# Performance work log

Hardware: AMD Instinct MI355X
Metric: run time of the kernel (lower is better)

The kernel has to match this reference:

```python
import jax, jax.numpy as jnp
import numpy as np

WIN = (8, 8)
NUM_HEADS = 6


def bchw_to_bnc(x, win):
    B, C, H, W = x.shape
    SH, SW = win
    oh, ow = H // SH, W // SW
    # B,C,oh,SH,ow,SW -> B,oh,ow,SH,SW,C -> (B*oh*ow, SH*SW, C)
    x = x.reshape(B, C, oh, SH, ow, SW)
    x = jnp.transpose(x, (0, 2, 4, 3, 5, 1))
    return x.reshape(B * oh * ow, SH * SW, C)


def bnc_to_bchw(x, out_shape, win):
    OB, OC, OH, OW = out_shape
    SH, SW = win
    oh, ow = OH // SH, OW // SW
    C = x.shape[-1]
    x = x.reshape(OB, oh, ow, SH, SW, C)
    x = jnp.transpose(x, (0, 5, 1, 3, 2, 4))
    return x.reshape(OB, C, OH, OW)


def setup_inputs() -> dict:
    key = jax.random.key(0)
    k1, k2, k3 = jax.random.split(key, 3)
    B, C, H, W = 4, 192, 384, 384
    x = jax.random.normal(k1, (B, C, H, W), dtype=jnp.float32)
    # MHA params: qkv_proj Linear(C, 3C), head_proj Linear(C, C)
    qkv_w = jax.random.normal(k2, (3 * C, C), dtype=jnp.float32) * 0.02
    qkv_b = jnp.zeros((3 * C,), dtype=jnp.float32)
    head_w = jax.random.normal(k3, (C, C), dtype=jnp.float32) * 0.02
    head_b = jnp.zeros((C,), dtype=jnp.float32)
    return {"x": x, "qkv_w": qkv_w, "qkv_b": qkv_b, "head_w": head_w, "head_b": head_b}


def reference(x, qkv_w, qkv_b, head_w, head_b):
    out_shape = x.shape
    C = x.shape[1]
    H = NUM_HEADS
    D = C // H  # head dim
    # window partition: (Bw, N, C) with N = 64
    t = bchw_to_bnc(x, WIN)
    # QKV projection
    qkv = t @ qkv_w.T + qkv_b  # (Bw, N, 3C)
    q, k, v = jnp.split(qkv, 3, axis=-1)
    Bw, N, _ = q.shape
    q = q.reshape(Bw, N, H, D).transpose(0, 2, 1, 3)  # bhnd
    k = k.reshape(Bw, N, H, D).transpose(0, 2, 1, 3)
    v = v.reshape(Bw, N, H, D).transpose(0, 2, 1, 3)
    scale = 1.0 / jnp.sqrt(jnp.asarray(D, dtype=q.dtype))
    scores = jnp.einsum('bhqd,bhkd->bhqk', q, k) * scale
    attn = jax.nn.softmax(scores, axis=-1)
    o = jnp.einsum('bhqk,bhkd->bhqd', attn, v)
    o = o.transpose(0, 2, 1, 3).reshape(Bw, N, C)
    o = o @ head_w.T + head_b
    return bnc_to_bchw(o, out_shape, WIN)
```

## Files before the change

kernel.cpp:

```cpp
#include <hip/hip_runtime.h>
#include <hip/hip_bf16.h>

typedef __attribute__((ext_vector_type(8))) short short8;
typedef __attribute__((ext_vector_type(4))) float f32x4;

#if __has_builtin(__builtin_amdgcn_exp2f)
#define EXP2F(x) __builtin_amdgcn_exp2f(x)
#else
#define EXP2F(x) exp2f(x)
#endif
#if __has_builtin(__builtin_amdgcn_rcpf)
#define RCPF(x) __builtin_amdgcn_rcpf(x)
#else
#define RCPF(x) (1.0f/(x))
#endif

#define SQ 208
#define SV 144

#define LDS_TOTAL 66048

__device__ __forceinline__ unsigned short f2bf(float f) {
    union { float f; unsigned u; } v; v.f = f;
    unsigned r = v.u + 0x7FFFu + ((v.u >> 16) & 1u);
    return (unsigned short)(r >> 16);
}
__device__ __forceinline__ unsigned pk2(float lo, float hi) {
    __hip_bfloat162 h = __float22bfloat162_rn(make_float2(lo, hi));
    union { __hip_bfloat162 h; unsigned u; } cv;
    cv.h = h;
    return cv.u;
}

__global__ void cvt_weights(const float* __restrict__ qw, const float* __restrict__ hw,
                            unsigned short* __restrict__ wq, unsigned short* __restrict__ wh) {
    int i = blockIdx.x * 256 + threadIdx.x;
    if (i < 576 * 192) wq[i] = f2bf(qw[i]);
    if (i < 192 * 192) wh[i] = f2bf(hw[i]);
}

__global__ __launch_bounds__(256, 2) void wmha(
    const float* __restrict__ x, const float* __restrict__ qkv_b,
    const float* __restrict__ head_b, const unsigned short* __restrict__ wq,
    const unsigned short* __restrict__ whc, float* __restrict__ out)
{
    extern __shared__ char smem[];
    char* const x_lds = smem;
    char* const o_lds = smem;
    char* const q_lds = smem + 25600;
    char* const k_lds = smem + 38912;
    char* const v_lds = smem + 52224;

    const int tid = threadIdx.x;
    const int ln  = tid & 15;
    const int hi4 = (tid >> 4) & 3;
    const int wid = tid >> 6;
    char* const p_scr = smem + 13312 + wid * 2304;

    const int bid  = blockIdx.x;
    const int widx = (bid & 7) * 1152 + (bid >> 3);
    const int b  = widx / 2304;
    const int rr = widx % 2304;
    const int oy = rr / 48, ox = rr % 48;
    const int row0 = oy * 8, col0 = ox * 8;

    auto ldwf = [&](int g, int mt, short8* wf) {
        const int hl = mt / 6, sec = (mt % 6) >> 1, e = mt & 1;
        const int r0 = sec * 192 + (3 * g + hl) * 32 + e * 16;
        #pragma unroll
        for (int kt = 0; kt < 6; ++kt)
            wf[kt] = *(const short8*)(wq + (r0 + ln) * 192 + kt * 32 + hi4 * 8);
    };

    short8 wf0[6];
    ldwf(0, wid, wf0);

    {
        const int tok = tid & 63;
        const int qd  = tid >> 6;
        const int y = tok >> 3, xx = tok & 7;
        const float* gp = x + ((size_t)(b * 192) * 384 + (row0 + y)) * 384 + (col0 + xx);
        char* wp = x_lds + tok * 400 + qd * 96;
        #pragma unroll
        for (int kk = 0; kk < 12; ++kk) {
            const int c = qd * 48 + kk * 4;
            float f0 = gp[(size_t)(c + 0) * 147456];
            float f1 = gp[(size_t)(c + 1) * 147456];
            float f2 = gp[(size_t)(c + 2) * 147456];
            float f3 = gp[(size_t)(c + 3) * 147456];
            uint2 u;
            u.x = pk2(f0, f1);
            u.y = pk2(f2, f3);
            *(uint2*)(wp + kk * 8) = u;
        }
    }
    __syncthreads();

    short8 bx[4][6];

    f32x4 acc[3][4];
    #pragma unroll
    for (int mm = 0; mm < 3; ++mm)
        #pragma unroll
        for (int nt = 0; nt < 4; ++nt)
            acc[mm][nt] = (f32x4){0.f, 0.f, 0.f, 0.f};

    const float SC2 = 0.25503417f;

    auto qkv_do = [&](int g, int mt, const short8* wf) {
        const int hl = mt / 6, sec = (mt % 6) >> 1, e = mt & 1;
        const int r0 = sec * 192 + (3 * g + hl) * 32 + e * 16;
        if (sec < 2) {
            char* dst = (sec == 0) ? q_lds : k_lds;
            const float4 bias = *(const float4*)(qkv_b + r0 + hi4 * 4);
            #pragma unroll
            for (int nt = 0; nt < 4; ++nt) {
                f32x4 a = {bias.x, bias.y, bias.z, bias.w};
                #pragma unroll
                for (int kt = 0; kt < 6; ++kt)
                    a = __builtin_amdgcn_mfma_f32_16x16x32_bf16(wf[kt], bx[nt][kt], a, 0, 0, 0);
                uint2 u;
                u.x = pk2(a[0], a[1]);
                u.y = pk2(a[2], a[3]);
                *(uint2*)(dst + (nt * 16 + ln) * SQ + hl * 64 + (e * 16 + hi4 * 4) * 2) = u;
            }
        } else {
            const float bv = qkv_b[r0 + ln];
            #pragma unroll
            for (int nt = 0; nt < 4; ++nt) {
                f32x4 a = {bv, bv, bv, bv};
                #pragma unroll
                for (int kt = 0; kt < 6; ++kt)
                    a = __builtin_amdgcn_mfma_f32_16x16x32_bf16(bx[nt][kt], wf[kt], a, 0, 0, 0);
                uint2 u;
                u.x = pk2(a[0], a[1]);
                u.y = pk2(a[2], a[3]);
                *(uint2*)(v_lds + (hl * 32 + e * 16 + ln) * SV + (nt * 16 + hi4 * 4) * 2) = u;
            }
        }
    };

    auto attn = [&](int g) {
        #pragma unroll
        for (int uu = 0; uu < 3; ++uu) {
            const int u = wid + uu * 4;
            const int hl = u >> 2, i0 = (u & 3) * 16;
            const short8 bq = *(const short8*)(q_lds + (i0 + ln) * SQ + hl * 64 + hi4 * 16);
            f32x4 s[4];
            #pragma unroll
            for (int kt = 0; kt < 4; ++kt) {
                const short8 ak = *(const short8*)(k_lds + (kt * 16 + ln) * SQ + hl * 64 + hi4 * 16);
                f32x4 z = {0.f, 0.f, 0.f, 0.f};
                s[kt] = __builtin_amdgcn_mfma_f32_16x16x32_bf16(ak, bq, z, 0, 0, 0);
            }
            float sum = 0.f;
            #pragma unroll
            for (int kt = 0; kt < 4; ++kt)
                #pragma unroll
                for (int r = 0; r < 4; ++r) {
                    s[kt][r] = EXP2F(s[kt][r] * SC2);
                    sum += s[kt][r];
                }
            sum += __shfl_xor(sum, 16);
            sum += __shfl_xor(sum, 32);
            const float rinv = RCPF(sum);
            #pragma unroll
            for (int kt = 0; kt < 4; ++kt) {
                uint2 u2;
                u2.x = pk2(s[kt][0], s[kt][1]);
                u2.y = pk2(s[kt][2], s[kt][3]);
                *(uint2*)(p_scr + ln * SV + kt * 32 + hi4 * 8) = u2;
            }
            short8 pf[2];
            #pragma unroll
            for (int kc = 0; kc < 2; ++kc)
                pf[kc] = *(const short8*)(p_scr + ln * SV + kc * 64 + hi4 * 16);
            #pragma unroll
            for (int dt = 0; dt < 2; ++dt) {
                f32x4 o = {0.f, 0.f, 0.f, 0.f};
                #pragma unroll
                for (int kc = 0; kc < 2; ++kc) {
                    const short8 av = *(const short8*)(v_lds + (hl * 32 + dt * 16 + ln) * SV + kc * 64 + hi4 * 16);
                    o = __builtin_amdgcn_mfma_f32_16x16x32_bf16(av, pf[kc], o, 0, 0, 0);
                }
                uint2 u2;
                u2.x = pk2(o[0] * rinv, o[1] * rinv);
                u2.y = pk2(o[2] * rinv, o[3] * rinv);
                *(uint2*)(o_lds + (i0 + ln) * SQ + hl * 64 + (dt * 16 + hi4 * 4) * 2) = u2;
            }
        }
    };

    auto proj = [&](int g) {
        short8 bo[4][3];
        #pragma unroll
        for (int nt = 0; nt < 4; ++nt)
            #pragma unroll
            for (int kt = 0; kt < 3; ++kt)
                bo[nt][kt] = *(const short8*)(o_lds + (nt * 16 + ln) * SQ + kt * 64 + hi4 * 16);
        #pragma unroll
        for (int mm = 0; mm < 3; ++mm) {
            const int c0 = (wid * 3 + mm) * 16;
            short8 af[3];
            #pragma unroll
            for (int kt = 0; kt < 3; ++kt)
                af[kt] = *(const short8*)(whc + (c0 + ln) * 192 + g * 96 + kt * 32 + hi4 * 8);
            #pragma unroll
            for (int nt = 0; nt < 4; ++nt)
                #pragma unroll
                for (int kt = 0; kt < 3; ++kt)
                    acc[mm][nt] = __builtin_amdgcn_mfma_f32_16x16x32_bf16(af[kt], bo[nt][kt], acc[mm][nt], 0, 0, 0);
        }
    };

    #pragma unroll
    for (int nt = 0; nt < 4; ++nt)
        #pragma unroll
        for (int kt = 0; kt < 6; ++kt)
            bx[nt][kt] = *(const short8*)(x_lds + (nt * 16 + ln) * 400 + kt * 64 + hi4 * 16);
    qkv_do(0, wid, wf0);
    for (int mt = wid + 4; mt < 18; mt += 4) {
        short8 wf[6];
        ldwf(0, mt, wf);
        qkv_do(0, mt, wf);
    }
    __syncthreads();
    attn(0);
    __syncthreads();
    proj(0);
    for (int mt = wid; mt < 18; mt += 4) {
        short8 wf[6];
        ldwf(1, mt, wf);
        qkv_do(1, mt, wf);
    }
    __syncthreads();
    attn(1);
    __syncthreads();
    proj(1);

    #pragma unroll
    for (int mm = 0; mm < 3; ++mm) {
        const int c0 = (wid * 3 + mm) * 16;
        const float4 hb = *(const float4*)(head_b + c0 + hi4 * 4);
        #pragma unroll
        for (int nt = 0; nt < 4; ++nt) {
            const int tt = nt * 16 + ln;
            const int y = tt >> 3, xx = tt & 7;
            float* op = out + ((size_t)(b * 192) * 384 + (row0 + y)) * 384 + (col0 + xx);
            op[(size_t)(c0 + hi4 * 4 + 0) * 147456] = acc[mm][nt][0] + hb.x;
            op[(size_t)(c0 + hi4 * 4 + 1) * 147456] = acc[mm][nt][1] + hb.y;
            op[(size_t)(c0 + hi4 * 4 + 2) * 147456] = acc[mm][nt][2] + hb.z;
            op[(size_t)(c0 + hi4 * 4 + 3) * 147456] = acc[mm][nt][3] + hb.w;
        }
    }
}

extern "C" void kernel_launch(void* const* d_in, const int* in_sizes, int n_in,
                              void* d_out, int out_size, void* d_ws, size_t ws_size,
                              hipStream_t stream) {
    const float* x      = (const float*)d_in[0];
    const float* qkv_w  = (const float*)d_in[1];
    const float* qkv_b  = (const float*)d_in[2];
    const float* head_w = (const float*)d_in[3];
    const float* head_b = (const float*)d_in[4];
    float* out = (float*)d_out;

    unsigned short* wq  = (unsigned short*)d_ws;
    unsigned short* whc = wq + 576 * 192;

    cvt_weights<<<432, 256, 0, stream>>>(qkv_w, head_w, wq, whc);

    hipFuncSetAttribute((const void*)wmha, hipFuncAttributeMaxDynamicSharedMemorySize, LDS_TOTAL);
    wmha<<<9216, 256, LDS_TOTAL, stream>>>(x, qkv_b, head_b, wq, whc, out);
}
```

Before: 541.9 us.

## Swizzle LDS tiles with XOR pattern and double-buffer QKV weight fragment loads

Applies an XOR swizzle to every LDS tile (x, q, k, v, o and the P scratch) and widens the q/k row stride to 256 bytes, so that fragment reads and writes fall on different banks. It also restructures the QKV loop to prefetch the next weight fragment into a second register set while the current MFMA tile runs, hiding global-load latency. The costs are extra LDS (about 72 KB per block), extra address arithmetic, and more registers, which could reduce occupancy under the two-block launch bound.

```diff
diff --git a/kernel.cpp b/kernel.cpp
--- a/kernel.cpp
+++ b/kernel.cpp
@@ -15,10 +15,10 @@
 #define RCPF(x) (1.0f/(x))
 #endif
 
-#define SQ 208
+#define SQ 256
 #define SV 144
 
-#define LDS_TOTAL 66048
+#define LDS_TOTAL 72192
 
 __device__ __forceinline__ unsigned short f2bf(float f) {
     union { float f; unsigned u; } v; v.f = f;
@@ -31,6 +31,7 @@
     cv.h = h;
     return cv.u;
 }
+__device__ __forceinline__ int SWZ(int row, int col) { return col ^ ((row & 7) << 4); }
 
 __global__ void cvt_weights(const float* __restrict__ qw, const float* __restrict__ hw,
                             unsigned short* __restrict__ wq, unsigned short* __restrict__ wh) {
@@ -48,14 +49,14 @@
     char* const x_lds = smem;
     char* const o_lds = smem;
     char* const q_lds = smem + 25600;
-    char* const k_lds = smem + 38912;
-    char* const v_lds = smem + 52224;
+    char* const k_lds = smem + 41984;
+    char* const v_lds = smem + 58368;
 
     const int tid = threadIdx.x;
     const int ln  = tid & 15;
     const int hi4 = (tid >> 4) & 3;
     const int wid = tid >> 6;
-    char* const p_scr = smem + 13312 + wid * 2304;
+    char* const p_scr = smem + 16384 + wid * 2304;
 
     const int bid  = blockIdx.x;
     const int widx = (bid & 7) * 1152 + (bid >> 3);
@@ -72,15 +73,15 @@
             wf[kt] = *(const short8*)(wq + (r0 + ln) * 192 + kt * 32 + hi4 * 8);
     };
 
-    short8 wf0[6];
-    ldwf(0, wid, wf0);
+    short8 wfP[6];
+    ldwf(0, wid, wfP);
 
     {
         const int tok = tid & 63;
         const int qd  = tid >> 6;
         const int y = tok >> 3, xx = tok & 7;
         const float* gp = x + ((size_t)(b * 192) * 384 + (row0 + y)) * 384 + (col0 + xx);
-        char* wp = x_lds + tok * 400 + qd * 96;
+        char* wp = x_lds + tok * 400;
         #pragma unroll
         for (int kk = 0; kk < 12; ++kk) {
             const int c = qd * 48 + kk * 4;
@@ -91,7 +92,7 @@
             uint2 u;
             u.x = pk2(f0, f1);
             u.y = pk2(f2, f3);
-            *(uint2*)(wp + kk * 8) = u;
+            *(uint2*)(wp + SWZ(tok, qd * 96 + kk * 8)) = u;
         }
     }
     __syncthreads();
@@ -122,7 +123,8 @@
                 uint2 u;
                 u.x = pk2(a[0], a[1]);
                 u.y = pk2(a[2], a[3]);
-                *(uint2*)(dst + (nt * 16 + ln) * SQ + hl * 64 + (e * 16 + hi4 * 4) * 2) = u;
+                const int t = nt * 16 + ln;
+                *(uint2*)(dst + t * SQ + SWZ(t, hl * 64 + e * 32 + hi4 * 8)) = u;
             }
         } else {
             const float bv = qkv_b[r0 + ln];
@@ -135,9 +137,24 @@
                 uint2 u;
                 u.x = pk2(a[0], a[1]);
                 u.y = pk2(a[2], a[3]);
-                *(uint2*)(v_lds + (hl * 32 + e * 16 + ln) * SV + (nt * 16 + hi4 * 4) * 2) = u;
-            }
-        }
+                const int row = hl * 32 + e * 16 + ln;
+                *(uint2*)(v_lds + row * SV + SWZ(row, nt * 32 + hi4 * 8)) = u;
+            }
+        }
+    };
+
+    auto qkv = [&](int g, short8 (&wfA)[6]) {
+        short8 wfB[6];
+        ldwf(g, wid + 4, wfB);
+        qkv_do(g, wid, wfA);
+        ldwf(g, wid + 8, wfA);
+        qkv_do(g, wid + 4, wfB);
+        ldwf(g, wid + 12, wfB);
+        qkv_do(g, wid + 8, wfA);
+        const bool extra = (wid < 2);
+        if (extra) ldwf(g, wid + 16, wfA);
+        qkv_do(g, wid + 12, wfB);
+        if (extra) qkv_do(g, wid + 16, wfA);
     };
 
     auto attn = [&](int g) {
@@ -145,11 +162,12 @@
         for (int uu = 0; uu < 3; ++uu) {
             const int u = wid + uu * 4;
             const int hl = u >> 2, i0 = (u & 3) * 16;
-            const short8 bq = *(const short8*)(q_lds + (i0 + ln) * SQ + hl * 64 + hi4 * 16);
+            const short8 bq = *(const short8*)(q_lds + (i0 + ln) * SQ + SWZ(i0 + ln, hl * 64 + hi4 * 16));
             f32x4 s[4];
             #pragma unroll
             for (int kt = 0; kt < 4; ++kt) {
-                const short8 ak = *(const short8*)(k_lds + (kt * 16 + ln) * SQ + hl * 64 + hi4 * 16);
+                const int rk = kt * 16 + ln;
+                const short8 ak = *(const short8*)(k_lds + rk * SQ + SWZ(rk, hl * 64 + hi4 * 16));
                 f32x4 z = {0.f, 0.f, 0.f, 0.f};
                 s[kt] = __builtin_amdgcn_mfma_f32_16x16x32_bf16(ak, bq, z, 0, 0, 0);
             }
@@ -169,24 +187,25 @@
                 uint2 u2;
                 u2.x = pk2(s[kt][0], s[kt][1]);
                 u2.y = pk2(s[kt][2], s[kt][3]);
-                *(uint2*)(p_scr + ln * SV + kt * 32 + hi4 * 8) = u2;
+                *(uint2*)(p_scr + ln * SV + SWZ(ln, kt * 32 + hi4 * 8)) = u2;
             }
             short8 pf[2];
             #pragma unroll
             for (int kc = 0; kc < 2; ++kc)
-                pf[kc] = *(const short8*)(p_scr + ln * SV + kc * 64 + hi4 * 16);
+                pf[kc] = *(const short8*)(p_scr + ln * SV + SWZ(ln, kc * 64 + hi4 * 16));
             #pragma unroll
             for (int dt = 0; dt < 2; ++dt) {
                 f32x4 o = {0.f, 0.f, 0.f, 0.f};
                 #pragma unroll
                 for (int kc = 0; kc < 2; ++kc) {
-                    const short8 av = *(const short8*)(v_lds + (hl * 32 + dt * 16 + ln) * SV + kc * 64 + hi4 * 16);
+                    const int rv = hl * 32 + dt * 16 + ln;
+                    const short8 av = *(const short8*)(v_lds + rv * SV + SWZ(rv, kc * 64 + hi4 * 16));
                     o = __builtin_amdgcn_mfma_f32_16x16x32_bf16(av, pf[kc], o, 0, 0, 0);
                 }
                 uint2 u2;
                 u2.x = pk2(o[0] * rinv, o[1] * rinv);
                 u2.y = pk2(o[2] * rinv, o[3] * rinv);
-                *(uint2*)(o_lds + (i0 + ln) * SQ + hl * 64 + (dt * 16 + hi4 * 4) * 2) = u2;
+                *(uint2*)(o_lds + (i0 + ln) * SQ + SWZ(i0 + ln, hl * 64 + dt * 32 + hi4 * 8)) = u2;
             }
         }
     };
@@ -196,8 +215,10 @@
         #pragma unroll
         for (int nt = 0; nt < 4; ++nt)
             #pragma unroll
-            for (int kt = 0; kt < 3; ++kt)
-                bo[nt][kt] = *(const short8*)(o_lds + (nt * 16 + ln) * SQ + kt * 64 + hi4 * 16);
+            for (int kt = 0; kt < 3; ++kt) {
+                const int t = nt * 16 + ln;
+                bo[nt][kt] = *(const short8*)(o_lds + t * SQ + SWZ(t, kt * 64 + hi4 * 16));
+            }
         #pragma unroll
         for (int mm = 0; mm < 3; ++mm) {
             const int c0 = (wid * 3 + mm) * 16;
@@ -217,22 +238,14 @@
     for (int nt = 0; nt < 4; ++nt)
         #pragma unroll
         for (int kt = 0; kt < 6; ++kt)
-            bx[nt][kt] = *(const short8*)(x_lds + (nt * 16 + ln) * 400 + kt * 64 + hi4 * 16);
-    qkv_do(0, wid, wf0);
-    for (int mt = wid + 4; mt < 18; mt += 4) {
-        short8 wf[6];
-        ldwf(0, mt, wf);
-        qkv_do(0, mt, wf);
-    }
+            bx[nt][kt] = *(const short8*)(x_lds + (nt * 16 + ln) * 400 + SWZ(nt * 16 + ln, kt * 64 + hi4 * 16));
+    qkv(0, wfP);
     __syncthreads();
     attn(0);
     __syncthreads();
     proj(0);
-    for (int mt = wid; mt < 18; mt += 4) {
-        short8 wf[6];
-        ldwf(1, mt, wf);
-        qkv_do(1, mt, wf);
-    }
+    ldwf(1, wid, wfP);
+    qkv(1, wfP);
     __syncthreads();
     attn(1);
     __syncthreads();
```

New measurement: 633.5 us. +16.9%, slower.

## Overlap second-group V projection with first-group attention using a double-buffered V tile

Applied to the files above, without the earlier changes.

Adds a second V buffer in LDS so the V-projection tiles for head group 1 can be computed during group 0's attention, interleaved between attention units. The remaining Q/K tiles for group 1 are computed after proj(0). The goal is to fill MFMA idle time during softmax and attention, and to balance work across waves. The cost is more LDS (79872 bytes instead of 66048), which may reduce how many blocks fit per CU, plus extra register pressure from holding the V weight fragments across the attention calls.

```diff
diff --git a/kernel.cpp b/kernel.cpp
--- a/kernel.cpp
+++ b/kernel.cpp
@@ -18,7 +18,7 @@
 #define SQ 208
 #define SV 144
 
-#define LDS_TOTAL 66048
+#define LDS_TOTAL 79872
 
 __device__ __forceinline__ unsigned short f2bf(float f) {
     union { float f; unsigned u; } v; v.f = f;
@@ -45,11 +45,12 @@
     const unsigned short* __restrict__ whc, float* __restrict__ out)
 {
     extern __shared__ char smem[];
-    char* const x_lds = smem;
-    char* const o_lds = smem;
-    char* const q_lds = smem + 25600;
-    char* const k_lds = smem + 38912;
-    char* const v_lds = smem + 52224;
+    char* const x_lds  = smem;
+    char* const o_lds  = smem;
+    char* const q_lds  = smem + 25600;
+    char* const k_lds  = smem + 38912;
+    char* const v0_lds = smem + 52224;
+    char* const v1_lds = smem + 66048;
 
     const int tid = threadIdx.x;
     const int ln  = tid & 15;
@@ -107,7 +108,7 @@
 
     const float SC2 = 0.25503417f;
 
-    auto qkv_do = [&](int g, int mt, const short8* wf) {
+    auto qkv_do = [&](int g, int mt, const short8* wf, char* vdst) {
         const int hl = mt / 6, sec = (mt % 6) >> 1, e = mt & 1;
         const int r0 = sec * 192 + (3 * g + hl) * 32 + e * 16;
         if (sec < 2) {
@@ -135,59 +136,56 @@
                 uint2 u;
                 u.x = pk2(a[0], a[1]);
                 u.y = pk2(a[2], a[3]);
-                *(uint2*)(v_lds + (hl * 32 + e * 16 + ln) * SV + (nt * 16 + hi4 * 4) * 2) = u;
-            }
-        }
-    };
-
-    auto attn = [&](int g) {
-        #pragma unroll
-        for (int uu = 0; uu < 3; ++uu) {
-            const int u = wid + uu * 4;
-            const int hl = u >> 2, i0 = (u & 3) * 16;
-            const short8 bq = *(const short8*)(q_lds + (i0 + ln) * SQ + hl * 64 + hi4 * 16);
-            f32x4 s[4];
-            #pragma unroll
-            for (int kt = 0; kt < 4; ++kt) {
-                const short8 ak = *(const short8*)(k_lds + (kt * 16 + ln) * SQ + hl * 64 + hi4 * 16);
-                f32x4 z = {0.f, 0.f, 0.f, 0.f};
-                s[kt] = __builtin_amdgcn_mfma_f32_16x16x32_bf16(ak, bq, z, 0, 0, 0);
-            }
-            float sum = 0.f;
-            #pragma unroll
-            for (int kt = 0; kt < 4; ++kt)
-                #pragma unroll
-                for (int r = 0; r < 4; ++r) {
-                    s[kt][r] = EXP2F(s[kt][r] * SC2);
-                    sum += s[kt][r];
-                }
-            sum += __shfl_xor(sum, 16);
-            sum += __shfl_xor(sum, 32);
-            const float rinv = RCPF(sum);
-            #pragma unroll
-            for (int kt = 0; kt < 4; ++kt) {
-                uint2 u2;
-                u2.x = pk2(s[kt][0], s[kt][1]);
-                u2.y = pk2(s[kt][2], s[kt][3]);
-                *(uint2*)(p_scr + ln * SV + kt * 32 + hi4 * 8) = u2;
-            }
-            short8 pf[2];
-            #pragma unroll
-            for (int kc = 0; kc < 2; ++kc)
-                pf[kc] = *(const short8*)(p_scr + ln * SV + kc * 64 + hi4 * 16);
-            #pragma unroll
-            for (int dt = 0; dt < 2; ++dt) {
-                f32x4 o = {0.f, 0.f, 0.f, 0.f};
-                #pragma unroll
-                for (int kc = 0; kc < 2; ++kc) {
-                    const short8 av = *(const short8*)(v_lds + (hl * 32 + dt * 16 + ln) * SV + kc * 64 + hi4 * 16);
-                    o = __builtin_amdgcn_mfma_f32_16x16x32_bf16(av, pf[kc], o, 0, 0, 0);
-                }
-                uint2 u2;
-                u2.x = pk2(o[0] * rinv, o[1] * rinv);
-                u2.y = pk2(o[2] * rinv, o[3] * rinv);
-                *(uint2*)(o_lds + (i0 + ln) * SQ + hl * 64 + (dt * 16 + hi4 * 4) * 2) = u2;
-            }
+                *(uint2*)(vdst + (hl * 32 + e * 16 + ln) * SV + (nt * 16 + hi4 * 4) * 2) = u;
+            }
+        }
+    };
+
+    auto attn_unit = [&](int g, int uu, const char* vbuf) {
+        const int u = wid + uu * 4;
+        const int hl = u >> 2, i0 = (u & 3) * 16;
+        const short8 bq = *(const short8*)(q_lds + (i0 + ln) * SQ + hl * 64 + hi4 * 16);
+        f32x4 s[4];
+        #pragma unroll
+        for (int kt = 0; kt < 4; ++kt) {
+            const short8 ak = *(const short8*)(k_lds + (kt * 16 + ln) * SQ + hl * 64 + hi4 * 16);
+            f32x4 z = {0.f, 0.f, 0.f, 0.f};
+            s[kt] = __builtin_amdgcn_mfma_f32_16x16x32_bf16(ak, bq, z, 0, 0, 0);
+        }
+        float sum = 0.f;
+        #pragma unroll
+        for (int kt = 0; kt < 4; ++kt)
+            #pragma unroll
+            for (int r = 0; r < 4; ++r) {
+                s[kt][r] = EXP2F(s[kt][r] * SC2);
+                sum += s[kt][r];
+            }
+        sum += __shfl_xor(sum, 16);
+        sum += __shfl_xor(sum, 32);
+        const float rinv = RCPF(sum);
+        #pragma unroll
+        for (int kt = 0; kt < 4; ++kt) {
+            uint2 u2;
+            u2.x = pk2(s[kt][0], s[kt][1]);
+            u2.y = pk2(s[kt][2], s[kt][3]);
+            *(uint2*)(p_scr + ln * SV + kt * 32 + hi4 * 8) = u2;
+        }
+        short8 pf[2];
+        #pragma unroll
+        for (int kc = 0; kc < 2; ++kc)
+            pf[kc] = *(const short8*)(p_scr + ln * SV + kc * 64 + hi4 * 16);
+        #pragma unroll
+        for (int dt = 0; dt < 2; ++dt) {
+            f32x4 o = {0.f, 0.f, 0.f, 0.f};
+            #pragma unroll
+            for (int kc = 0; kc < 2; ++kc) {
+                const short8 av = *(const short8*)(vbuf + (hl * 32 + dt * 16 + ln) * SV + kc * 64 + hi4 * 16);
+                o = __builtin_amdgcn_mfma_f32_16x16x32_bf16(av, pf[kc], o, 0, 0, 0);
+            }
+            uint2 u2;
+            u2.x = pk2(o[0] * rinv, o[1] * rinv);
+            u2.y = pk2(o[2] * rinv, o[3] * rinv);
+            *(uint2*)(o_lds + (i0 + ln) * SQ + hl * 64 + (dt * 16 + hi4 * 4) * 2) = u2;
         }
     };
 
@@ -218,23 +216,40 @@
         #pragma unroll
         for (int kt = 0; kt < 6; ++kt)
             bx[nt][kt] = *(const short8*)(x_lds + (nt * 16 + ln) * 400 + kt * 64 + hi4 * 16);
-    qkv_do(0, wid, wf0);
+    qkv_do(0, wid, wf0, v0_lds);
     for (int mt = wid + 4; mt < 18; mt += 4) {
         short8 wf[6];
         ldwf(0, mt, wf);
-        qkv_do(0, mt, wf);
-    }
-    __syncthreads();
-    attn(0);
-    __syncthreads();
+        qkv_do(0, mt, wf, v0_lds);
+    }
+    __syncthreads();
+
+    {
+        const int vt0 = (wid < 2) ? 4 + wid : 8 + wid;
+        const int vt1 = 16 + wid;
+        short8 wv0[6], wv1[6];
+        ldwf(1, vt0, wv0);
+        if (wid < 2) ldwf(1, vt1, wv1);
+        attn_unit(0, 0, v0_lds);
+        qkv_do(1, vt0, wv0, v1_lds);
+        attn_unit(0, 1, v0_lds);
+        if (wid < 2) qkv_do(1, vt1, wv1, v1_lds);
+        attn_unit(0, 2, v0_lds);
+    }
+    __syncthreads();
+
     proj(0);
-    for (int mt = wid; mt < 18; mt += 4) {
+    for (int j = 0; j < 3; ++j) {
+        const int mt = j * 6 + wid;
         short8 wf[6];
         ldwf(1, mt, wf);
-        qkv_do(1, mt, wf);
-    }
-    __syncthreads();
-    attn(1);
+        qkv_do(1, mt, wf, v1_lds);
+    }
+    __syncthreads();
+
+    attn_unit(1, 0, v1_lds);
+    attn_unit(1, 1, v1_lds);
+    attn_unit(1, 2, v1_lds);
     __syncthreads();
     proj(1);
 
```

New measurement: 557.6 us. +2.9%, slower.
